# Kernel optimization log

Measured on AMD Instinct MI355X. Metric: run time of the kernel, lower is better.

Reference implementation:

```python
import jax, jax.numpy as jnp
import numpy as np

DIM = 192
HEADS = 6
WIN = (2, 6, 12)          # (pl, lat, lon)
TOW = 64                  # type_of_windows = (8//2)*(96//6)
N_TOK = WIN[0] * WIN[1] * WIN[2]            # 144
TABLE_ROWS = WIN[0]**2 * WIN[1]**2 * (2 * WIN[2] - 1)  # 3312


def calc_position_bias_indices(size):
    pl, la, lo = size
    plq = np.arange(pl); plk = -np.arange(pl) * pl
    laq = np.arange(la); lak = -np.arange(la) * la
    lon = np.arange(lo)
    gq = np.stack(np.meshgrid(plq, laq, lon, indexing='ij'))  # [3,pl,la,lo]
    gk = np.stack(np.meshgrid(plk, lak, lon, indexing='ij'))
    fq = gq.reshape(3, -1)
    fk = gk.reshape(3, -1)
    d = fq[:, :, None] - fk[:, None, :]          # [3,N,N]
    d = np.transpose(d, (1, 2, 0)).copy()
    d[:, :, 2] += lo - 1
    d[:, :, 1] *= 2 * lo - 1
    d[:, :, 0] *= (2 * lo - 1) * la * la
    return d.sum(-1)                              # [N,N]


def setup_inputs() -> dict:
    key = jax.random.key(0)
    ks = jax.random.split(key, 7)
    B_, nW, N, C = 15, TOW, N_TOK, DIM
    x = jax.random.normal(ks[0], (B_, nW, N, C), jnp.float32)
    mask = jax.random.normal(ks[1], (15, nW, N, N), jnp.float32)  # nLon=15
    qkv_w = jax.random.normal(ks[2], (3 * C, C), jnp.float32) * 0.02
    qkv_b = jnp.zeros((3 * C,), jnp.float32)
    table = jax.random.normal(ks[3], (TABLE_ROWS, TOW, HEADS), jnp.float32) * 0.02
    proj_w = jax.random.normal(ks[4], (C, C), jnp.float32) * 0.02
    proj_b = jnp.zeros((C,), jnp.float32)
    pos_index = jnp.asarray(calc_position_bias_indices(WIN), jnp.int32)  # [N,N]
    return {"x": x, "mask": mask, "qkv_w": qkv_w, "qkv_b": qkv_b,
            "table": table, "proj_w": proj_w, "proj_b": proj_b,
            "pos_index": pos_index}


def reference(x, mask, qkv_w, qkv_b, table, proj_w, proj_b, pos_index):
    B_, nW, N, C = x.shape
    h = HEADS
    hd = C // h
    scale = hd ** -0.5
    # qkv projection -> (3, B_, h, nW, N, hd)
    qkv = (jnp.einsum('bwnc,dc->bwnd', x, qkv_w) + qkv_b)
    qkv = qkv.reshape(B_, nW, N, 3, h, hd).transpose(3, 0, 4, 1, 2, 5)
    q, k, v = qkv[0] * scale, qkv[1], qkv[2]
    attn = jnp.einsum('bhwqd,bhwkd->bhwqk', q, k)      # [B_,h,nW,N,N]
    # gather earth position bias: [N,N,tow,h] -> [h,tow,N,N]
    bias = table[pos_index.reshape(-1)].reshape(N, N, nW, h)
    bias = bias.transpose(3, 2, 0, 1)
    attn = attn + bias[None]
    nLon = mask.shape[0]
    attn = attn.reshape(B_ // nLon, nLon, h, nW, N, N) + mask[None, :, None]
    attn = attn.reshape(B_, h, nW, N, N)
    attn = jax.nn.softmax(attn, axis=-1)
    out = jnp.einsum('bhwqk,bhwkd->bhwqd', attn, v)
    out = out.transpose(0, 2, 3, 1, 4).reshape(B_, nW, N, C)
    return jnp.einsum('bwnc,dc->bwnd', out, proj_w) + proj_b
```

## Files before the change

### kernel.cpp

```cpp
#include <hip/hip_runtime.h>

#define HEADS 6
#define N_TOK 144
#define DIM   192
#define NW    64
#define NB    15
#define NBW   (NB * NW)
#define CHUNK 480

typedef __attribute__((ext_vector_type(8))) short bf16x8;
typedef __attribute__((ext_vector_type(4))) float f32x4;

#define MFMA(a, b, c) __builtin_amdgcn_mfma_f32_16x16x32_bf16(a, b, c, 0, 0, 0)

static __device__ __forceinline__ short f2bf(float f) {
    union { float f; unsigned u; } v; v.f = f;
    unsigned r = v.u + 0x7FFFu + ((v.u >> 16) & 1u);
    return (short)(r >> 16);
}
static __device__ __forceinline__ float bf2f(short s) {
    union { unsigned u; float f; } v;
    v.u = ((unsigned)(unsigned short)s) << 16;
    return v.f;
}
static __device__ __forceinline__ unsigned pk2(float a, float b) {
    return (unsigned)(unsigned short)f2bf(a) |
           ((unsigned)(unsigned short)f2bf(b) << 16);
}

__global__ __launch_bounds__(256)
void bias_k(const float* __restrict__ table, const int* __restrict__ pos_index,
            short* __restrict__ bias_bf) {
    const int t = blockIdx.x;
    for (int e = threadIdx.x; e < N_TOK * N_TOK; e += 256) {
        int idx = pos_index[e];
        bias_bf[(long)t * (N_TOK * N_TOK) + e] = f2bf(table[(long)idx * 384 + t]);
    }
}

__global__ __launch_bounds__(256)
void cvt_k(const float* __restrict__ w, short* __restrict__ o, int n) {
    int i = blockIdx.x * 256 + threadIdx.x;
    if (i < n) o[i] = f2bf(w[i]);
}

__global__ __launch_bounds__(256)
void cvtx_k(const float* __restrict__ x, short* __restrict__ xb, int n4) {
    int i = blockIdx.x * 256 + threadIdx.x;
    if (i < n4) {
        float4 f = ((const float4*)x)[i];
        short4 s = { f2bf(f.x), f2bf(f.y), f2bf(f.z), f2bf(f.w) };
        ((short4*)xb)[i] = s;
    }
}

__global__ __launch_bounds__(576)
void qkvs_k(const short* __restrict__ xb, const short* __restrict__ qkvw_bf,
            const float* __restrict__ qkv_b, short* __restrict__ qkv_out) {
    __shared__ short wlds[192 * 200];

    const int sel = blockIdx.x % 3;
    const int bwL = blockIdx.x / 3;
    const int tid = threadIdx.x;

    for (int u = tid * 8; u < 192 * 192; u += 576 * 8) {
        int r = u / 192, c = u - r * 192;
        *(bf16x8*)&wlds[r * 200 + c] = *(const bf16x8*)&qkvw_bf[sel * 36864 + u];
    }
    __syncthreads();

    const int wid = tid >> 6, lane = tid & 63, lq = lane & 15, lg = lane >> 4;
    const int mg = wid / 3, ng = wid % 3;
    const short* xrow = xb + (long)bwL * N_TOK * DIM;

    f32x4 acc[3][4] = {};
    for (int ks = 0; ks < 6; ++ks) {
        const int k0 = ks * 32 + 8 * lg;
        bf16x8 av[3], bv[4];
        #pragma unroll
        for (int mt = 0; mt < 3; ++mt)
            av[mt] = *(const bf16x8*)&xrow[(mg * 48 + mt * 16 + lq) * DIM + k0];
        #pragma unroll
        for (int nt = 0; nt < 4; ++nt)
            bv[nt] = *(const bf16x8*)&wlds[(ng * 64 + nt * 16 + lq) * 200 + k0];
        #pragma unroll
        for (int mt = 0; mt < 3; ++mt)
            #pragma unroll
            for (int nt = 0; nt < 4; ++nt)
                acc[mt][nt] = MFMA(av[mt], bv[nt], acc[mt][nt]);
    }
    __syncthreads();

    const float scale = 0.17677669529663687f;
    #pragma unroll
    for (int nt = 0; nt < 4; ++nt) {
        const int cd = ng * 64 + nt * 16 + lq;
        const float bb = qkv_b[sel * 192 + cd];
        #pragma unroll
        for (int mt = 0; mt < 3; ++mt)
            #pragma unroll
            for (int i = 0; i < 4; ++i) {
                int row = mg * 48 + mt * 16 + 4 * lg + i;
                float v = acc[mt][nt][i] + bb;
                if (sel == 0) v *= scale;
                wlds[row * 200 + cd] = f2bf(v);
            }
    }
    __syncthreads();

    short* ob = qkv_out + (long)bwL * 6 * 3 * 4608 + (long)sel * 4608;
    #pragma unroll
    for (int j = 0; j < 6; ++j) {
        int u = (j * 576 + tid) * 8;
        int h = u / 4608, rem = u - h * 4608;
        int row = rem >> 5, e = rem & 31;
        *(bf16x8*)&ob[(long)h * 3 * 4608 + rem] =
            *(const bf16x8*)&wlds[row * 200 + h * 32 + e];
    }
}

__global__ __launch_bounds__(576)
void attn3_k(const short* __restrict__ qkv, const short* __restrict__ bias_bf,
             const float* __restrict__ mask, short* __restrict__ tmp, int bw0) {
    __shared__ short vlds[32 * 152];
    __shared__ short pws[9 * 16 * 40];

    const int bwL = blockIdx.x;
    const int bwG = bw0 + bwL;
    const int tid = threadIdx.x;
    const int lane = tid & 63, lq = lane & 15, lg = lane >> 4;
    const int wid = tid >> 6;
    const int q = wid * 16 + lq;
    const int w = bwG & 63;

    const float* mp = mask + (long)bwG * (N_TOK * N_TOK) + q * N_TOK + 4 * lg;
    float4 mreg[9];
    #pragma unroll
    for (int nt = 0; nt < 9; ++nt) mreg[nt] = *(const float4*)&mp[nt * 16];

    short* pw = pws + wid * 16 * 40;
    short* tb = tmp + (long)bwL * N_TOK * DIM + q * DIM;
    const f32x4 zf = {};
    const bf16x8 zb = {};

    #pragma unroll 1
    for (int h = 0; h < HEADS; ++h) {
        const short* qb = qkv + ((long)(bwL * 6 + h) * 3) * 4608;
        const short* kb = qb + 4608;
        const short* vb = qb + 9216;

        __syncthreads();
        {
            int j = tid >> 2, e0 = (tid & 3) * 8;
            bf16x8 vv = *(const bf16x8*)&vb[j * 32 + e0];
            #pragma unroll
            for (int u = 0; u < 8; ++u) vlds[(e0 + u) * 152 + j] = vv[u];
        }
        __syncthreads();

        bf16x8 bq = *(const bf16x8*)&qb[q * 32 + 8 * lg];
        f32x4 lgt[9];
        #pragma unroll
        for (int nt = 0; nt < 9; ++nt) {
            bf16x8 ak = *(const bf16x8*)&kb[(nt * 16 + lq) * 32 + 8 * lg];
            lgt[nt] = MFMA(ak, bq, zf);
        }

        const short* bp = bias_bf + (long)(w * 6 + h) * (N_TOK * N_TOK)
                        + q * N_TOK + 4 * lg;
        #pragma unroll
        for (int nt = 0; nt < 9; ++nt) {
            short4 bs = *(const short4*)&bp[nt * 16];
            lgt[nt][0] += bf2f(bs.x) + mreg[nt].x;
            lgt[nt][1] += bf2f(bs.y) + mreg[nt].y;
            lgt[nt][2] += bf2f(bs.z) + mreg[nt].z;
            lgt[nt][3] += bf2f(bs.w) + mreg[nt].w;
        }

        float m = lgt[0][0];
        #pragma unroll
        for (int nt = 0; nt < 9; ++nt)
            #pragma unroll
            for (int i = 0; i < 4; ++i) m = fmaxf(m, lgt[nt][i]);
        m = fmaxf(m, __shfl_xor(m, 16));
        m = fmaxf(m, __shfl_xor(m, 32));
        float s = 0.f;
        #pragma unroll
        for (int nt = 0; nt < 9; ++nt)
            #pragma unroll
            for (int i = 0; i < 4; ++i) {
                float p = __expf(lgt[nt][i] - m);
                lgt[nt][i] = p;
                s += p;
            }
        s += __shfl_xor(s, 16);
        s += __shfl_xor(s, 32);
        const float inv = 1.f / s;

        f32x4 o[2] = {};
        #pragma unroll
        for (int kt = 0; kt < 5; ++kt) {
            const int nt0 = 2 * kt;
            *(unsigned*)&pw[lq * 40 + 4 * lg]     = pk2(lgt[nt0][0], lgt[nt0][1]);
            *(unsigned*)&pw[lq * 40 + 4 * lg + 2] = pk2(lgt[nt0][2], lgt[nt0][3]);
            if (kt < 4) {
                const int nt1 = nt0 + 1;
                *(unsigned*)&pw[lq * 40 + 16 + 4 * lg]     = pk2(lgt[nt1][0], lgt[nt1][1]);
                *(unsigned*)&pw[lq * 40 + 16 + 4 * lg + 2] = pk2(lgt[nt1][2], lgt[nt1][3]);
            }
            bf16x8 bpf = *(const bf16x8*)&pw[lq * 40 + 8 * lg];
            #pragma unroll
            for (int et = 0; et < 2; ++et) {
                bf16x8 av = *(const bf16x8*)&vlds[(et * 16 + lq) * 152 + kt * 32 + 8 * lg];
                bf16x8 aa = av, bb = bpf;
                if (kt == 4 && lg >= 2) { aa = zb; bb = zb; }
                o[et] = MFMA(aa, bb, o[et]);
            }
        }

        #pragma unroll
        for (int et = 0; et < 2; ++et) {
            short4 sx = { f2bf(o[et][0] * inv), f2bf(o[et][1] * inv),
                          f2bf(o[et][2] * inv), f2bf(o[et][3] * inv) };
            *(short4*)&tb[h * 32 + et * 16 + 4 * lg] = sx;
        }
    }
}

__global__ __launch_bounds__(192)
void proj_k(const short* __restrict__ tmp, const short* __restrict__ pwt,
            const float* __restrict__ proj_b, float* __restrict__ out, int bw0) {
    const int bid = blockIdx.x;
    const int mthird = bid % 3;
    const int bwL = bid / 3;
    const int bwG = bw0 + bwL;
    const int tid = threadIdx.x;
    const int wid = tid >> 6, lane = tid & 63, lq = lane & 15, lg = lane >> 4;
    const int m0 = (mthird * 3 + wid) * 16;
    const short* tb = tmp + (long)bwL * N_TOK * DIM;

    f32x4 acc[12] = {};
    for (int ks = 0; ks < 6; ++ks) {
        const int k0 = ks * 32 + 8 * lg;
        bf16x8 a = *(const bf16x8*)&tb[(m0 + lq) * DIM + k0];
        #pragma unroll
        for (int nt = 0; nt < 12; ++nt) {
            bf16x8 b = *(const bf16x8*)&pwt[(nt * 16 + lq) * DIM + k0];
            acc[nt] = MFMA(a, b, acc[nt]);
        }
    }
    float* ob = out + (long)bwG * N_TOK * DIM;
    #pragma unroll
    for (int nt = 0; nt < 12; ++nt) {
        float pb = proj_b[nt * 16 + lq];
        #pragma unroll
        for (int i = 0; i < 4; ++i)
            ob[(m0 + 4 * lg + i) * DIM + nt * 16 + lq] = acc[nt][i] + pb;
    }
}

extern "C" void kernel_launch(void* const* d_in, const int* in_sizes, int n_in,
                              void* d_out, int out_size, void* d_ws, size_t ws_size,
                              hipStream_t stream) {
    const float* x        = (const float*)d_in[0];
    const float* mask     = (const float*)d_in[1];
    const float* qkv_w    = (const float*)d_in[2];
    const float* qkv_b    = (const float*)d_in[3];
    const float* table    = (const float*)d_in[4];
    const float* proj_w   = (const float*)d_in[5];
    const float* proj_b   = (const float*)d_in[6];
    const int*   pos_index= (const int*)d_in[7];
    float* out = (float*)d_out;

    short* bias_bf  = (short*)d_ws;
    short* projw_bf = bias_bf + (size_t)384 * N_TOK * N_TOK;
    short* qkvw_bf  = projw_bf + 36864;
    short* xbf_ws   = qkvw_bf + 110592;
    short* tmp_ws   = xbf_ws;
    short* qkv_ws   = xbf_ws + (size_t)CHUNK * N_TOK * DIM;

    bias_k<<<384, 256, 0, stream>>>(table, pos_index, bias_bf);
    cvt_k<<<144, 256, 0, stream>>>(proj_w, projw_bf, DIM * DIM);
    cvt_k<<<432, 256, 0, stream>>>(qkv_w, qkvw_bf, 3 * DIM * DIM);

    const int n4 = CHUNK * N_TOK * DIM / 4;
    for (int c = 0; c < 2; ++c) {
        const int bw0 = c * CHUNK;
        cvtx_k<<<(n4 + 255) / 256, 256, 0, stream>>>(
            x + (long)bw0 * N_TOK * DIM, xbf_ws, n4);
        qkvs_k<<<CHUNK * 3, 576, 0, stream>>>(xbf_ws, qkvw_bf, qkv_b, qkv_ws);
        attn3_k<<<CHUNK, 576, 0, stream>>>(qkv_ws, bias_bf, mask, tmp_ws, bw0);
        proj_k<<<CHUNK * 3, 192, 0, stream>>>(tmp_ws, projw_bf, proj_b, out, bw0);
    }
}
```

Measured before the change: 440.0 us.

## Fuse x conversion and QKV projection into attention kernel, drop chunking

Merges the x-to-bf16 conversion, the QKV GEMM and the attention into one kernel per window. Each wave computes its q/k/v rows per head straight from fp32 x held in registers and stages K and V through LDS. This removes the round trips of bf16 x and the qkv intermediate through global memory, and the separate launches. The two-chunk loop is also dropped so attention and proj each run in a single launch. In exchange, each block rereads the QKV weights from global/L2 per head, does more synchronisation, and loads the mask per head instead of holding it in registers.

```diff
diff --git a/kernel.cpp b/kernel.cpp
--- a/kernel.cpp
+++ b/kernel.cpp
@@ -6,7 +6,6 @@
 #define NW    64
 #define NB    15
 #define NBW   (NB * NW)
-#define CHUNK 480
 
 typedef __attribute__((ext_vector_type(8))) short bf16x8;
 typedef __attribute__((ext_vector_type(4))) float f32x4;
@@ -44,125 +43,87 @@
     if (i < n) o[i] = f2bf(w[i]);
 }
 
-__global__ __launch_bounds__(256)
-void cvtx_k(const float* __restrict__ x, short* __restrict__ xb, int n4) {
-    int i = blockIdx.x * 256 + threadIdx.x;
-    if (i < n4) {
-        float4 f = ((const float4*)x)[i];
-        short4 s = { f2bf(f.x), f2bf(f.y), f2bf(f.z), f2bf(f.w) };
-        ((short4*)xb)[i] = s;
-    }
-}
-
-__global__ __launch_bounds__(576)
-void qkvs_k(const short* __restrict__ xb, const short* __restrict__ qkvw_bf,
-            const float* __restrict__ qkv_b, short* __restrict__ qkv_out) {
-    __shared__ short wlds[192 * 200];
-
-    const int sel = blockIdx.x % 3;
-    const int bwL = blockIdx.x / 3;
-    const int tid = threadIdx.x;
-
-    for (int u = tid * 8; u < 192 * 192; u += 576 * 8) {
-        int r = u / 192, c = u - r * 192;
-        *(bf16x8*)&wlds[r * 200 + c] = *(const bf16x8*)&qkvw_bf[sel * 36864 + u];
-    }
-    __syncthreads();
-
-    const int wid = tid >> 6, lane = tid & 63, lq = lane & 15, lg = lane >> 4;
-    const int mg = wid / 3, ng = wid % 3;
-    const short* xrow = xb + (long)bwL * N_TOK * DIM;
-
-    f32x4 acc[3][4] = {};
-    for (int ks = 0; ks < 6; ++ks) {
-        const int k0 = ks * 32 + 8 * lg;
-        bf16x8 av[3], bv[4];
-        #pragma unroll
-        for (int mt = 0; mt < 3; ++mt)
-            av[mt] = *(const bf16x8*)&xrow[(mg * 48 + mt * 16 + lq) * DIM + k0];
-        #pragma unroll
-        for (int nt = 0; nt < 4; ++nt)
-            bv[nt] = *(const bf16x8*)&wlds[(ng * 64 + nt * 16 + lq) * 200 + k0];
-        #pragma unroll
-        for (int mt = 0; mt < 3; ++mt)
-            #pragma unroll
-            for (int nt = 0; nt < 4; ++nt)
-                acc[mt][nt] = MFMA(av[mt], bv[nt], acc[mt][nt]);
-    }
-    __syncthreads();
-
-    const float scale = 0.17677669529663687f;
-    #pragma unroll
-    for (int nt = 0; nt < 4; ++nt) {
-        const int cd = ng * 64 + nt * 16 + lq;
-        const float bb = qkv_b[sel * 192 + cd];
-        #pragma unroll
-        for (int mt = 0; mt < 3; ++mt)
-            #pragma unroll
-            for (int i = 0; i < 4; ++i) {
-                int row = mg * 48 + mt * 16 + 4 * lg + i;
-                float v = acc[mt][nt][i] + bb;
-                if (sel == 0) v *= scale;
-                wlds[row * 200 + cd] = f2bf(v);
-            }
-    }
-    __syncthreads();
-
-    short* ob = qkv_out + (long)bwL * 6 * 3 * 4608 + (long)sel * 4608;
-    #pragma unroll
-    for (int j = 0; j < 6; ++j) {
-        int u = (j * 576 + tid) * 8;
-        int h = u / 4608, rem = u - h * 4608;
-        int row = rem >> 5, e = rem & 31;
-        *(bf16x8*)&ob[(long)h * 3 * 4608 + rem] =
-            *(const bf16x8*)&wlds[row * 200 + h * 32 + e];
-    }
-}
-
-__global__ __launch_bounds__(576)
-void attn3_k(const short* __restrict__ qkv, const short* __restrict__ bias_bf,
-             const float* __restrict__ mask, short* __restrict__ tmp, int bw0) {
+__global__ __launch_bounds__(576, 4)
+void fused_k(const float* __restrict__ x, const short* __restrict__ qkvw_bf,
+             const float* __restrict__ qkv_b, const short* __restrict__ bias_bf,
+             const float* __restrict__ mask, short* __restrict__ tmp) {
+    __shared__ short klds[N_TOK * 40];
     __shared__ short vlds[32 * 152];
     __shared__ short pws[9 * 16 * 40];
 
-    const int bwL = blockIdx.x;
-    const int bwG = bw0 + bwL;
+    const int bw  = blockIdx.x;
     const int tid = threadIdx.x;
     const int lane = tid & 63, lq = lane & 15, lg = lane >> 4;
     const int wid = tid >> 6;
-    const int q = wid * 16 + lq;
-    const int w = bwG & 63;
-
-    const float* mp = mask + (long)bwG * (N_TOK * N_TOK) + q * N_TOK + 4 * lg;
-    float4 mreg[9];
-    #pragma unroll
-    for (int nt = 0; nt < 9; ++nt) mreg[nt] = *(const float4*)&mp[nt * 16];
+    const int m0 = wid * 16;
+    const int q  = m0 + lq;
+    const int w  = bw & 63;
+    const float scale = 0.17677669529663687f;
+
+    bf16x8 af[6];
+    {
+        const float* xg = x + ((long)bw * N_TOK + q) * DIM;
+        #pragma unroll
+        for (int ks = 0; ks < 6; ++ks) {
+            const float4* p = (const float4*)&xg[ks * 32 + 8 * lg];
+            float4 f0 = p[0], f1 = p[1];
+            bf16x8 a;
+            a[0]=f2bf(f0.x); a[1]=f2bf(f0.y); a[2]=f2bf(f0.z); a[3]=f2bf(f0.w);
+            a[4]=f2bf(f1.x); a[5]=f2bf(f1.y); a[6]=f2bf(f1.z); a[7]=f2bf(f1.w);
+            af[ks] = a;
+        }
+    }
 
     short* pw = pws + wid * 16 * 40;
-    short* tb = tmp + (long)bwL * N_TOK * DIM + q * DIM;
+    short* tb = tmp + ((long)bw * N_TOK + q) * DIM;
+    const float* mp = mask + (long)bw * (N_TOK * N_TOK) + q * N_TOK + 4 * lg;
     const f32x4 zf = {};
     const bf16x8 zb = {};
 
     #pragma unroll 1
     for (int h = 0; h < HEADS; ++h) {
-        const short* qb = qkv + ((long)(bwL * 6 + h) * 3) * 4608;
-        const short* kb = qb + 4608;
-        const short* vb = qb + 9216;
+        f32x4 acc[3][2] = {};
+        #pragma unroll
+        for (int sel = 0; sel < 3; ++sel) {
+            const short* wb = qkvw_bf + ((long)sel * 192 + h * 32) * 192;
+            #pragma unroll
+            for (int ks = 0; ks < 6; ++ks) {
+                #pragma unroll
+                for (int nt = 0; nt < 2; ++nt) {
+                    bf16x8 b = *(const bf16x8*)&wb[(nt * 16 + lq) * 192 + ks * 32 + 8 * lg];
+                    acc[sel][nt] = MFMA(af[ks], b, acc[sel][nt]);
+                }
+            }
+        }
+
+        #pragma unroll
+        for (int nt = 0; nt < 2; ++nt) {
+            float bb = qkv_b[h * 32 + nt * 16 + lq];
+            #pragma unroll
+            for (int i = 0; i < 4; ++i)
+                pw[(4 * lg + i) * 40 + nt * 16 + lq] =
+                    f2bf((acc[0][nt][i] + bb) * scale);
+        }
 
         __syncthreads();
-        {
-            int j = tid >> 2, e0 = (tid & 3) * 8;
-            bf16x8 vv = *(const bf16x8*)&vb[j * 32 + e0];
-            #pragma unroll
-            for (int u = 0; u < 8; ++u) vlds[(e0 + u) * 152 + j] = vv[u];
+
+        #pragma unroll
+        for (int nt = 0; nt < 2; ++nt) {
+            float bk = qkv_b[192 + h * 32 + nt * 16 + lq];
+            float bv = qkv_b[384 + h * 32 + nt * 16 + lq];
+            #pragma unroll
+            for (int i = 0; i < 4; ++i) {
+                klds[(m0 + 4 * lg + i) * 40 + nt * 16 + lq] = f2bf(acc[1][nt][i] + bk);
+                vlds[(nt * 16 + lq) * 152 + m0 + 4 * lg + i] = f2bf(acc[2][nt][i] + bv);
+            }
         }
         __syncthreads();
 
-        bf16x8 bq = *(const bf16x8*)&qb[q * 32 + 8 * lg];
+        bf16x8 bq = *(const bf16x8*)&pw[lq * 40 + 8 * lg];
         f32x4 lgt[9];
         #pragma unroll
         for (int nt = 0; nt < 9; ++nt) {
-            bf16x8 ak = *(const bf16x8*)&kb[(nt * 16 + lq) * 32 + 8 * lg];
+            bf16x8 ak = *(const bf16x8*)&klds[(nt * 16 + lq) * 40 + 8 * lg];
             lgt[nt] = MFMA(ak, bq, zf);
         }
 
@@ -171,10 +132,11 @@
         #pragma unroll
         for (int nt = 0; nt < 9; ++nt) {
             short4 bs = *(const short4*)&bp[nt * 16];
-            lgt[nt][0] += bf2f(bs.x) + mreg[nt].x;
-            lgt[nt][1] += bf2f(bs.y) + mreg[nt].y;
-            lgt[nt][2] += bf2f(bs.z) + mreg[nt].z;
-            lgt[nt][3] += bf2f(bs.w) + mreg[nt].w;
+            float4 mf = *(const float4*)&mp[nt * 16];
+            lgt[nt][0] += bf2f(bs.x) + mf.x;
+            lgt[nt][1] += bf2f(bs.y) + mf.y;
+            lgt[nt][2] += bf2f(bs.z) + mf.z;
+            lgt[nt][3] += bf2f(bs.w) + mf.w;
         }
 
         float m = lgt[0][0];
@@ -229,15 +191,14 @@
 
 __global__ __launch_bounds__(192)
 void proj_k(const short* __restrict__ tmp, const short* __restrict__ pwt,
-            const float* __restrict__ proj_b, float* __restrict__ out, int bw0) {
+            const float* __restrict__ proj_b, float* __restrict__ out) {
     const int bid = blockIdx.x;
     const int mthird = bid % 3;
-    const int bwL = bid / 3;
-    const int bwG = bw0 + bwL;
+    const int bw = bid / 3;
     const int tid = threadIdx.x;
     const int wid = tid >> 6, lane = tid & 63, lq = lane & 15, lg = lane >> 4;
     const int m0 = (mthird * 3 + wid) * 16;
-    const short* tb = tmp + (long)bwL * N_TOK * DIM;
+    const short* tb = tmp + (long)bw * N_TOK * DIM;
 
     f32x4 acc[12] = {};
     for (int ks = 0; ks < 6; ++ks) {
@@ -249,7 +210,7 @@
             acc[nt] = MFMA(a, b, acc[nt]);
         }
     }
-    float* ob = out + (long)bwG * N_TOK * DIM;
+    float* ob = out + (long)bw * N_TOK * DIM;
     #pragma unroll
     for (int nt = 0; nt < 12; ++nt) {
         float pb = proj_b[nt * 16 + lq];
@@ -275,21 +236,12 @@
     short* bias_bf  = (short*)d_ws;
     short* projw_bf = bias_bf + (size_t)384 * N_TOK * N_TOK;
     short* qkvw_bf  = projw_bf + 36864;
-    short* xbf_ws   = qkvw_bf + 110592;
-    short* tmp_ws   = xbf_ws;
-    short* qkv_ws   = xbf_ws + (size_t)CHUNK * N_TOK * DIM;
+    short* tmp_ws   = qkvw_bf + 110592;
 
     bias_k<<<384, 256, 0, stream>>>(table, pos_index, bias_bf);
     cvt_k<<<144, 256, 0, stream>>>(proj_w, projw_bf, DIM * DIM);
     cvt_k<<<432, 256, 0, stream>>>(qkv_w, qkvw_bf, 3 * DIM * DIM);
 
-    const int n4 = CHUNK * N_TOK * DIM / 4;
-    for (int c = 0; c < 2; ++c) {
-        const int bw0 = c * CHUNK;
-        cvtx_k<<<(n4 + 255) / 256, 256, 0, stream>>>(
-            x + (long)bw0 * N_TOK * DIM, xbf_ws, n4);
-        qkvs_k<<<CHUNK * 3, 576, 0, stream>>>(xbf_ws, qkvw_bf, qkv_b, qkv_ws);
-        attn3_k<<<CHUNK, 576, 0, stream>>>(qkv_ws, bias_bf, mask, tmp_ws, bw0);
-        proj_k<<<CHUNK * 3, 192, 0, stream>>>(tmp_ws, projw_bf, proj_b, out, bw0);
-    }
-}
+    fused_k<<<NBW, 576, 0, stream>>>(x, qkvw_bf, qkv_b, bias_bf, mask, tmp_ws);
+    proj_k<<<NBW * 3, 192, 0, stream>>>(tmp_ws, projw_bf, proj_b, out);
+}
```

After: 523.5 us. +19.0%, slower.

## Split attention per head across blocks and pre-transpose V in QKV kernel

Applied to the files above, without the earlier changes.

The attention kernel now launches one block per (window, head) pair instead of looping over six heads inside one block, and uses a swizzled block index. The QKV kernel writes Q/K to one buffer and V already transposed to a separate buffer, so the attention kernel loads V into LDS with vector copies instead of scalar transposing stores. The goal is more parallelism and less serial per-block work and synchronisation. The cost is that the mask row is re-read from memory once per head instead of being held in registers across heads.

```diff
diff --git a/kernel.cpp b/kernel.cpp
--- a/kernel.cpp
+++ b/kernel.cpp
@@ -56,7 +56,8 @@
 
 __global__ __launch_bounds__(576)
 void qkvs_k(const short* __restrict__ xb, const short* __restrict__ qkvw_bf,
-            const float* __restrict__ qkv_b, short* __restrict__ qkv_out) {
+            const float* __restrict__ qkv_b, short* __restrict__ qk_ws,
+            short* __restrict__ vT_ws) {
     __shared__ short wlds[192 * 200];
 
     const int sel = blockIdx.x % 3;
@@ -92,138 +93,159 @@
     __syncthreads();
 
     const float scale = 0.17677669529663687f;
-    #pragma unroll
-    for (int nt = 0; nt < 4; ++nt) {
-        const int cd = ng * 64 + nt * 16 + lq;
-        const float bb = qkv_b[sel * 192 + cd];
-        #pragma unroll
-        for (int mt = 0; mt < 3; ++mt)
+
+    if (sel < 2) {
+        #pragma unroll
+        for (int nt = 0; nt < 4; ++nt) {
+            const int cd = ng * 64 + nt * 16 + lq;
+            const float bb = qkv_b[sel * 192 + cd];
             #pragma unroll
-            for (int i = 0; i < 4; ++i) {
-                int row = mg * 48 + mt * 16 + 4 * lg + i;
-                float v = acc[mt][nt][i] + bb;
-                if (sel == 0) v *= scale;
-                wlds[row * 200 + cd] = f2bf(v);
-            }
-    }
-    __syncthreads();
-
-    short* ob = qkv_out + (long)bwL * 6 * 3 * 4608 + (long)sel * 4608;
-    #pragma unroll
-    for (int j = 0; j < 6; ++j) {
-        int u = (j * 576 + tid) * 8;
-        int h = u / 4608, rem = u - h * 4608;
-        int row = rem >> 5, e = rem & 31;
-        *(bf16x8*)&ob[(long)h * 3 * 4608 + rem] =
-            *(const bf16x8*)&wlds[row * 200 + h * 32 + e];
+            for (int mt = 0; mt < 3; ++mt)
+                #pragma unroll
+                for (int i = 0; i < 4; ++i) {
+                    int row = mg * 48 + mt * 16 + 4 * lg + i;
+                    float v = acc[mt][nt][i] + bb;
+                    if (sel == 0) v *= scale;
+                    wlds[row * 200 + cd] = f2bf(v);
+                }
+        }
+        __syncthreads();
+        short* ob = qk_ws + (long)bwL * 6 * 2 * 4608 + (long)sel * 4608;
+        #pragma unroll
+        for (int j = 0; j < 6; ++j) {
+            int u = (j * 576 + tid) * 8;
+            int h = u / 4608, rem = u - h * 4608;
+            int row = rem >> 5, e = rem & 31;
+            *(bf16x8*)&ob[(long)h * 2 * 4608 + rem] =
+                *(const bf16x8*)&wlds[row * 200 + h * 32 + e];
+        }
+    } else {
+        #pragma unroll
+        for (int nt = 0; nt < 4; ++nt) {
+            const int cd = ng * 64 + nt * 16 + lq;
+            const float bb = qkv_b[2 * 192 + cd];
+            #pragma unroll
+            for (int mt = 0; mt < 3; ++mt)
+                #pragma unroll
+                for (int i = 0; i < 4; ++i) {
+                    int row = mg * 48 + mt * 16 + 4 * lg + i;
+                    wlds[cd * 152 + row] = f2bf(acc[mt][nt][i] + bb);
+                }
+        }
+        __syncthreads();
+        short* ob = vT_ws + (long)bwL * 6 * 4608;
+        #pragma unroll
+        for (int j = 0; j < 6; ++j) {
+            int u = (j * 576 + tid) * 8;
+            int h = u / 4608, rem = u - h * 4608;
+            int e = rem / 144, row0 = rem - e * 144;
+            *(bf16x8*)&ob[(long)h * 4608 + e * 144 + row0] =
+                *(const bf16x8*)&wlds[(h * 32 + e) * 152 + row0];
+        }
     }
 }
 
 __global__ __launch_bounds__(576)
-void attn3_k(const short* __restrict__ qkv, const short* __restrict__ bias_bf,
-             const float* __restrict__ mask, short* __restrict__ tmp, int bw0) {
+void attn2v_k(const short* __restrict__ qk_ws, const short* __restrict__ vT_ws,
+              const short* __restrict__ bias_bf, const float* __restrict__ mask,
+              short* __restrict__ tmp, int bw0) {
     __shared__ short vlds[32 * 152];
     __shared__ short pws[9 * 16 * 40];
 
-    const int bwL = blockIdx.x;
+    const int p = blockIdx.x;
+    const int l = (p & 7) * 360 + (p >> 3);
+    const int h   = l % HEADS;
+    const int bwL = l / HEADS;
     const int bwG = bw0 + bwL;
     const int tid = threadIdx.x;
     const int lane = tid & 63, lq = lane & 15, lg = lane >> 4;
     const int wid = tid >> 6;
-    const int q = wid * 16 + lq;
-    const int w = bwG & 63;
-
+    const int m0 = wid * 16;
+    const int q  = m0 + lq;
+    const int w  = bwG & 63;
+
+    {
+        const short* vsrc = vT_ws + (long)(bwL * 6 + h) * 4608;
+        int e = tid / 18, k0 = (tid % 18) * 8;
+        bf16x8 v = *(const bf16x8*)&vsrc[e * N_TOK + k0];
+        *(bf16x8*)&vlds[e * 152 + k0] = v;
+    }
+    __syncthreads();
+
+    const short* qb = qk_ws + (long)(bwL * 6 + h) * 2 * 4608;
+    const short* kb = qb + 4608;
+
+    const f32x4 zf = {};
+    bf16x8 bq = *(const bf16x8*)&qb[q * 32 + 8 * lg];
+    f32x4 lgt[9];
+    #pragma unroll
+    for (int nt = 0; nt < 9; ++nt) {
+        bf16x8 ak = *(const bf16x8*)&kb[(nt * 16 + lq) * 32 + 8 * lg];
+        lgt[nt] = MFMA(ak, bq, zf);
+    }
+
+    const short* bp = bias_bf + (long)(w * 6 + h) * (N_TOK * N_TOK)
+                    + q * N_TOK + 4 * lg;
     const float* mp = mask + (long)bwG * (N_TOK * N_TOK) + q * N_TOK + 4 * lg;
-    float4 mreg[9];
-    #pragma unroll
-    for (int nt = 0; nt < 9; ++nt) mreg[nt] = *(const float4*)&mp[nt * 16];
+    #pragma unroll
+    for (int nt = 0; nt < 9; ++nt) {
+        short4 bs = *(const short4*)&bp[nt * 16];
+        float4 mf = *(const float4*)&mp[nt * 16];
+        lgt[nt][0] += bf2f(bs.x) + mf.x;
+        lgt[nt][1] += bf2f(bs.y) + mf.y;
+        lgt[nt][2] += bf2f(bs.z) + mf.z;
+        lgt[nt][3] += bf2f(bs.w) + mf.w;
+    }
+
+    float m = lgt[0][0];
+    #pragma unroll
+    for (int nt = 0; nt < 9; ++nt)
+        #pragma unroll
+        for (int i = 0; i < 4; ++i) m = fmaxf(m, lgt[nt][i]);
+    m = fmaxf(m, __shfl_xor(m, 16));
+    m = fmaxf(m, __shfl_xor(m, 32));
+    float s = 0.f;
+    #pragma unroll
+    for (int nt = 0; nt < 9; ++nt)
+        #pragma unroll
+        for (int i = 0; i < 4; ++i) {
+            float pe = __expf(lgt[nt][i] - m);
+            lgt[nt][i] = pe;
+            s += pe;
+        }
+    s += __shfl_xor(s, 16);
+    s += __shfl_xor(s, 32);
+    const float inv = 1.f / s;
 
     short* pw = pws + wid * 16 * 40;
-    short* tb = tmp + (long)bwL * N_TOK * DIM + q * DIM;
-    const f32x4 zf = {};
+    f32x4 o[2] = {};
     const bf16x8 zb = {};
-
-    #pragma unroll 1
-    for (int h = 0; h < HEADS; ++h) {
-        const short* qb = qkv + ((long)(bwL * 6 + h) * 3) * 4608;
-        const short* kb = qb + 4608;
-        const short* vb = qb + 9216;
-
-        __syncthreads();
-        {
-            int j = tid >> 2, e0 = (tid & 3) * 8;
-            bf16x8 vv = *(const bf16x8*)&vb[j * 32 + e0];
-            #pragma unroll
-            for (int u = 0; u < 8; ++u) vlds[(e0 + u) * 152 + j] = vv[u];
-        }
-        __syncthreads();
-
-        bf16x8 bq = *(const bf16x8*)&qb[q * 32 + 8 * lg];
-        f32x4 lgt[9];
-        #pragma unroll
-        for (int nt = 0; nt < 9; ++nt) {
-            bf16x8 ak = *(const bf16x8*)&kb[(nt * 16 + lq) * 32 + 8 * lg];
-            lgt[nt] = MFMA(ak, bq, zf);
-        }
-
-        const short* bp = bias_bf + (long)(w * 6 + h) * (N_TOK * N_TOK)
-                        + q * N_TOK + 4 * lg;
-        #pragma unroll
-        for (int nt = 0; nt < 9; ++nt) {
-            short4 bs = *(const short4*)&bp[nt * 16];
-            lgt[nt][0] += bf2f(bs.x) + mreg[nt].x;
-            lgt[nt][1] += bf2f(bs.y) + mreg[nt].y;
-            lgt[nt][2] += bf2f(bs.z) + mreg[nt].z;
-            lgt[nt][3] += bf2f(bs.w) + mreg[nt].w;
-        }
-
-        float m = lgt[0][0];
-        #pragma unroll
-        for (int nt = 0; nt < 9; ++nt)
-            #pragma unroll
-            for (int i = 0; i < 4; ++i) m = fmaxf(m, lgt[nt][i]);
-        m = fmaxf(m, __shfl_xor(m, 16));
-        m = fmaxf(m, __shfl_xor(m, 32));
-        float s = 0.f;
-        #pragma unroll
-        for (int nt = 0; nt < 9; ++nt)
-            #pragma unroll
-            for (int i = 0; i < 4; ++i) {
-                float p = __expf(lgt[nt][i] - m);
-                lgt[nt][i] = p;
-                s += p;
-            }
-        s += __shfl_xor(s, 16);
-        s += __shfl_xor(s, 32);
-        const float inv = 1.f / s;
-
-        f32x4 o[2] = {};
-        #pragma unroll
-        for (int kt = 0; kt < 5; ++kt) {
-            const int nt0 = 2 * kt;
-            *(unsigned*)&pw[lq * 40 + 4 * lg]     = pk2(lgt[nt0][0], lgt[nt0][1]);
-            *(unsigned*)&pw[lq * 40 + 4 * lg + 2] = pk2(lgt[nt0][2], lgt[nt0][3]);
-            if (kt < 4) {
-                const int nt1 = nt0 + 1;
-                *(unsigned*)&pw[lq * 40 + 16 + 4 * lg]     = pk2(lgt[nt1][0], lgt[nt1][1]);
-                *(unsigned*)&pw[lq * 40 + 16 + 4 * lg + 2] = pk2(lgt[nt1][2], lgt[nt1][3]);
-            }
-            bf16x8 bpf = *(const bf16x8*)&pw[lq * 40 + 8 * lg];
-            #pragma unroll
-            for (int et = 0; et < 2; ++et) {
-                bf16x8 av = *(const bf16x8*)&vlds[(et * 16 + lq) * 152 + kt * 32 + 8 * lg];
-                bf16x8 aa = av, bb = bpf;
-                if (kt == 4 && lg >= 2) { aa = zb; bb = zb; }
-                o[et] = MFMA(aa, bb, o[et]);
-            }
-        }
-
+    #pragma unroll
+    for (int kt = 0; kt < 5; ++kt) {
+        const int nt0 = 2 * kt;
+        *(unsigned*)&pw[lq * 40 + 4 * lg]     = pk2(lgt[nt0][0], lgt[nt0][1]);
+        *(unsigned*)&pw[lq * 40 + 4 * lg + 2] = pk2(lgt[nt0][2], lgt[nt0][3]);
+        if (kt < 4) {
+            const int nt1 = nt0 + 1;
+            *(unsigned*)&pw[lq * 40 + 16 + 4 * lg]     = pk2(lgt[nt1][0], lgt[nt1][1]);
+            *(unsigned*)&pw[lq * 40 + 16 + 4 * lg + 2] = pk2(lgt[nt1][2], lgt[nt1][3]);
+        }
+        bf16x8 bpf = *(const bf16x8*)&pw[lq * 40 + 8 * lg];
         #pragma unroll
         for (int et = 0; et < 2; ++et) {
-            short4 sx = { f2bf(o[et][0] * inv), f2bf(o[et][1] * inv),
-                          f2bf(o[et][2] * inv), f2bf(o[et][3] * inv) };
-            *(short4*)&tb[h * 32 + et * 16 + 4 * lg] = sx;
-        }
+            bf16x8 av = *(const bf16x8*)&vlds[(et * 16 + lq) * 152 + kt * 32 + 8 * lg];
+            bf16x8 aa = av, bb = bpf;
+            if (kt == 4 && lg >= 2) { aa = zb; bb = zb; }
+            o[et] = MFMA(aa, bb, o[et]);
+        }
+    }
+
+    short* tb = tmp + ((long)bwL * N_TOK + q) * DIM + h * 32;
+    #pragma unroll
+    for (int et = 0; et < 2; ++et) {
+        short4 sx = { f2bf(o[et][0] * inv), f2bf(o[et][1] * inv),
+                      f2bf(o[et][2] * inv), f2bf(o[et][3] * inv) };
+        *(short4*)&tb[et * 16 + 4 * lg] = sx;
     }
 }
 
@@ -277,7 +299,8 @@
     short* qkvw_bf  = projw_bf + 36864;
     short* xbf_ws   = qkvw_bf + 110592;
     short* tmp_ws   = xbf_ws;
-    short* qkv_ws   = xbf_ws + (size_t)CHUNK * N_TOK * DIM;
+    short* qk_ws    = xbf_ws + (size_t)CHUNK * N_TOK * DIM;
+    short* vT_ws    = qk_ws + (size_t)CHUNK * 6 * 2 * 4608;
 
     bias_k<<<384, 256, 0, stream>>>(table, pos_index, bias_bf);
     cvt_k<<<144, 256, 0, stream>>>(proj_w, projw_bf, DIM * DIM);
@@ -288,8 +311,10 @@
         const int bw0 = c * CHUNK;
         cvtx_k<<<(n4 + 255) / 256, 256, 0, stream>>>(
             x + (long)bw0 * N_TOK * DIM, xbf_ws, n4);
-        qkvs_k<<<CHUNK * 3, 576, 0, stream>>>(xbf_ws, qkvw_bf, qkv_b, qkv_ws);
-        attn3_k<<<CHUNK, 576, 0, stream>>>(qkv_ws, bias_bf, mask, tmp_ws, bw0);
+        qkvs_k<<<CHUNK * 3, 576, 0, stream>>>(xbf_ws, qkvw_bf, qkv_b,
+                                              qk_ws, vT_ws);
+        attn2v_k<<<CHUNK * 6, 576, 0, stream>>>(qk_ws, vT_ws, bias_bf, mask,
+                                                tmp_ws, bw0);
         proj_k<<<CHUNK * 3, 192, 0, stream>>>(tmp_ws, projw_bf, proj_b, out, bw0);
     }
 }
```

New measurement: 445.1 us. Within noise of the previous version (+1.2%).
